# Optimization experiments

Hardware: AMD Instinct MI355X
Metric: run time of the kernel (lower is better)

## Reference

```python
import jax, jax.numpy as jnp
import numpy as np
from jax import lax

DN = ('NCHW', 'OIHW', 'NCHW')


def _conv(x, w, stride, pad):
    return lax.conv_general_dilated(
        x, w, window_strides=(stride, stride),
        padding=((pad, pad), (pad, pad)), dimension_numbers=DN)


def _deconv(x, w):
    # PyTorch ConvTranspose2d(k=4, s=2, p=1): input dilation 2, pad k-1-p=2 -> doubles H,W
    return lax.conv_general_dilated(
        x, w, window_strides=(1, 1), padding=((2, 2), (2, 2)),
        lhs_dilation=(2, 2), dimension_numbers=DN)


def setup_inputs() -> dict:
    key = jax.random.key(0)
    ks = jax.random.split(key, 10)
    B, H, W = 32, 256, 256
    K, E, HID = 512, 64, 128
    s = 0.05
    return {
        'x': jax.random.normal(ks[0], (B, 3, H, W), jnp.float32),
        'enc_w1': jax.random.normal(ks[1], (HID, 3, 4, 4), jnp.float32) * s,
        'enc_b1': jnp.zeros((HID,), jnp.float32),
        'enc_w2': jax.random.normal(ks[2], (E, HID, 4, 4), jnp.float32) * s,
        'enc_b2': jnp.zeros((E,), jnp.float32),
        'dec_w1': jax.random.normal(ks[3], (HID, E, 4, 4), jnp.float32) * s,
        'dec_b1': jnp.zeros((HID,), jnp.float32),
        'dec_w2': jax.random.normal(ks[4], (3, HID, 4, 4), jnp.float32) * s,
        'dec_b2': jnp.zeros((3,), jnp.float32),
        'codebook': jax.random.uniform(ks[5], (K, E), jnp.float32,
                                       minval=-1.0 / K, maxval=1.0 / K),
    }


def reference(x, enc_w1, enc_b1, enc_w2, enc_b2,
              dec_w1, dec_b1, dec_w2, dec_b2, codebook):
    h1 = jax.nn.relu(_conv(x, enc_w1, 2, 1) + enc_b1[None, :, None, None])
    z = _conv(h1, enc_w2, 2, 1) + enc_b2[None, :, None, None]  # [b, e, h, w]

    # ---- vector quantization (faithful to torch reshape order) ----
    b, c, h, w = z.shape
    e = codebook.shape[1]
    zf = z.reshape(b, -1, e)  # [b, n, e] with n = c*h*w/e (c == e -> n = h*w)
    # squared L2 to all codes via quadratic expansion (argmin identical to sqrt-dist)
    d2 = ((zf * zf).sum(-1)[..., None]
          - 2.0 * jnp.einsum('bne,ke->bnk', zf, codebook)
          + (codebook * codebook).sum(-1)[None, None, :])  # [b, n, K]
    idx = jnp.argmin(d2, axis=-1)                            # [b, n]
    z_q = codebook[idx].transpose(0, 2, 1).reshape(-1, e, h, w)  # [b, e, h, w]

    # ---- straight-through estimator ----
    z_q_st = z + lax.stop_gradient(z_q - z)

    d1 = jax.nn.relu(_deconv(z_q_st, dec_w1) + dec_b1[None, :, None, None])
    out = _deconv(d1, dec_w2) + dec_b2[None, :, None, None]
    return out
```

## Files before the change

### kernel.cpp

```cpp
#include <hip/hip_runtime.h>


__device__ int g_isbf;

__device__ __forceinline__ float ldin(const void* p, long long i, int isbf) {
  if (isbf) {
    unsigned v = ((const unsigned short*)p)[i];
    return __uint_as_float(v << 16);
  }
  return ((const float*)p)[i];
}

__device__ __forceinline__ unsigned short f2bf(float f) {
  unsigned u = __float_as_uint(f);
  u += 0x7FFFu + ((u >> 16) & 1u);
  return (unsigned short)(u >> 16);
}

__device__ __forceinline__ float tree64(const float* a) {
  float m[16], u[8], v[4];
#pragma unroll
  for (int l = 0; l < 16; ++l)
    m[l] = __fadd_rn(__fadd_rn(a[l], a[l + 16]), __fadd_rn(a[l + 32], a[l + 48]));
#pragma unroll
  for (int l = 0; l < 8; ++l) u[l] = __fadd_rn(m[l], m[l + 8]);
#pragma unroll
  for (int l = 0; l < 4; ++l) v[l] = __fadd_rn(u[l], u[l + 4]);
  return __fadd_rn(__fadd_rn(v[0], v[2]), __fadd_rn(v[1], v[3]));
}

#define O_W1F   0
#define O_W2T   6144
#define O_DWT2  137216
#define O_DW2T2 268288
#define O_CB    276480
#define O_CN3   309248
#define O_B1    310272
#define O_B2    310400
#define O_DB1   310464
#define O_DB2   310592
#define HDRF    310608
#define PF      1048576
#define PERB    1064960

__global__ void VQVAE_31525059952911_kernel() {}

__global__ __launch_bounds__(256) void k_detect(const unsigned* __restrict__ x) {
  __shared__ int red[256];
  int t = threadIdx.x;
  int cnt = 0;
  for (int i = t; i < 2048; i += 256) {
    unsigned h = x[i] & 0xFFFFu;
    unsigned e = (h >> 7) & 0xFFu;
    if (e >= 100u && e <= 140u) cnt++;
  }
  red[t] = cnt;
  __syncthreads();
  for (int s = 128; s > 0; s >>= 1) {
    if (t < s) red[t] += red[t + s];
    __syncthreads();
  }
  if (t == 0) g_isbf = (red[0] > 1024) ? 1 : 0;
}

__global__ __launch_bounds__(256) void k_prep(
    const void* __restrict__ w1, const void* __restrict__ b1,
    const void* __restrict__ w2, const void* __restrict__ b2,
    const void* __restrict__ dw1, const void* __restrict__ db1,
    const void* __restrict__ dw2, const void* __restrict__ db2,
    const void* __restrict__ cb, float* __restrict__ ws) {
  const int isbf = g_isbf;
  int id = blockIdx.x * 256 + threadIdx.x;
  if (id < 6144) { ws[O_W1F + id] = ldin(w1, id, isbf); return; }
  id -= 6144;
  if (id < 131072) {
    int ci = id >> 10, tap = (id >> 6) & 15, o = id & 63;
    ws[O_W2T + id] = ldin(w2, (o * 128 + ci) * 16 + tap, isbf);
    return;
  }
  id -= 131072;
  if (id < 131072) {
    int r = id & 3, tap = (id >> 2) & 15, ci = (id >> 6) & 63, q = id >> 12;
    ws[O_DWT2 + id] = ldin(dw1, ((q * 4 + r) * 64 + ci) * 16 + tap, isbf);
    return;
  }
  id -= 131072;
  if (id < 8192) {
    int o = id & 3, tap = (id >> 2) & 15, cil = (id >> 6) & 3, cc = id >> 8;
    ws[O_DW2T2 + id] = (o < 3) ? ldin(dw2, (o * 128 + cc * 4 + cil) * 16 + tap, isbf) : 0.f;
    return;
  }
  id -= 8192;
  if (id < 32768) { ws[O_CB + id] = ldin(cb, id, isbf); return; }
  id -= 32768;
  if (id < 512) {
    float q[64];
    for (int d = 0; d < 64; ++d) {
      float v = ldin(cb, id * 64 + d, isbf);
      q[d] = __fmul_rn(v, v);
    }
    ws[O_CN3 + id] = tree64(q);
    return;
  }
  id -= 512;
  if (id < 128) { ws[O_B1 + id] = ldin(b1, id, isbf); return; }
  id -= 128;
  if (id < 64) { ws[O_B2 + id] = ldin(b2, id, isbf); return; }
  id -= 64;
  if (id < 128) { ws[O_DB1 + id] = ldin(db1, id, isbf); return; }
  id -= 4 + 124;
  if (id < 4) { ws[O_DB2 + id] = (id < 3) ? ldin(db2, id, isbf) : 0.f; return; }
}

__global__ __launch_bounds__(256) void k_pproj(
    const void* __restrict__ dw1, const void* __restrict__ cb,
    float* __restrict__ P) {
  __shared__ float cbs[64];
  const int isbf = g_isbf;
  const int t = threadIdx.x;
  const int k = blockIdx.x;
  if (t < 64) cbs[t] = ldin(cb, (long long)k * 64 + t, isbf);
  __syncthreads();
  const int oc = t & 127;
  const int th = t >> 7;
  float acc[8];
#pragma unroll
  for (int j = 0; j < 8; ++j) acc[j] = 0.f;
  for (int ci = 0; ci < 64; ++ci) {
    const float v = cbs[ci];
    const long long base = ((long long)oc * 64 + ci) * 16 + th * 8;
    float wv[8];
    if (isbf) {
      const uint4 raw = *(const uint4*)((const unsigned short*)dw1 + base);
      wv[0] = __uint_as_float((raw.x & 0xFFFFu) << 16);
      wv[1] = __uint_as_float(raw.x & 0xFFFF0000u);
      wv[2] = __uint_as_float((raw.y & 0xFFFFu) << 16);
      wv[3] = __uint_as_float(raw.y & 0xFFFF0000u);
      wv[4] = __uint_as_float((raw.z & 0xFFFFu) << 16);
      wv[5] = __uint_as_float(raw.z & 0xFFFF0000u);
      wv[6] = __uint_as_float((raw.w & 0xFFFFu) << 16);
      wv[7] = __uint_as_float(raw.w & 0xFFFF0000u);
    } else {
      const float4 a = *(const float4*)((const float*)dw1 + base);
      const float4 b = *(const float4*)((const float*)dw1 + base + 4);
      wv[0] = a.x; wv[1] = a.y; wv[2] = a.z; wv[3] = a.w;
      wv[4] = b.x; wv[5] = b.y; wv[6] = b.z; wv[7] = b.w;
    }
#pragma unroll
    for (int j = 0; j < 8; ++j) acc[j] = fmaf(v, wv[j], acc[j]);
  }
#pragma unroll
  for (int j = 0; j < 8; ++j)
    P[(k << 11) + ((th * 8 + j) << 7) + oc] = acc[j];
}

__global__ __launch_bounds__(256) void k_enc(
    const void* __restrict__ x, const float* __restrict__ w1f,
    const float* __restrict__ w2t, const float* __restrict__ b1,
    const float* __restrict__ b2, float* __restrict__ z, int b0) {
  __shared__ float x_s[3][38][38];
  __shared__ float w2_s[8192];
  __shared__ float w1c_s[384];
  __shared__ float h1_s[8][18][18];
  __shared__ float b2_s[64];
  __shared__ float b1c_s[8];
  const int isbf = g_isbf;
  const int t = threadIdx.x;
  const int bz = blockIdx.z, y0 = blockIdx.y * 8, x0 = blockIdx.x * 8;
  const long long xbase = (long long)(b0 + bz) * 3 * 65536;
  for (int i = t; i < 4332; i += 256) {
    int ci = i / 1444, rem = i % 1444, lr = rem / 38, lc = rem % 38;
    int iy = 4 * y0 - 3 + lr, ix = 4 * x0 - 3 + lc;
    float v = 0.f;
    if (iy >= 0 && iy < 256 && ix >= 0 && ix < 256)
      v = ldin(x, xbase + (long long)ci * 65536 + iy * 256 + ix, isbf);
    x_s[ci][lr][lc] = v;
  }
  if (t < 64) b2_s[t] = b2[t];
  const int co0 = (t >> 4) * 4;
  const int pg = t & 15, py = pg & 7, px0 = (pg >> 3) * 4;
  float acc[4][4];
#pragma unroll
  for (int c = 0; c < 4; ++c)
#pragma unroll
    for (int u = 0; u < 4; ++u) acc[c][u] = 0.f;
  for (int cc = 0; cc < 16; ++cc) {
    __syncthreads();
    for (int i = t; i < 8192; i += 256) w2_s[i] = w2t[cc * 8192 + i];
    for (int i = t; i < 384; i += 256) w1c_s[i] = w1f[cc * 384 + i];
    if (t < 8) b1c_s[t] = b1[cc * 8 + t];
    __syncthreads();
    for (int j = t; j < 2592; j += 256) {
      int c = j / 324, rem = j % 324, ly = rem / 18, lx = rem % 18;
      int hy = 2 * y0 - 1 + ly, hx = 2 * x0 - 1 + lx;
      float v = 0.f;
      if (hy >= 0 && hy < 128 && hx >= 0 && hx < 128) {
        const float* wc = &w1c_s[c * 48];
        float a = 0.f;
        for (int ci = 0; ci < 3; ++ci) {
#pragma unroll
          for (int ky = 0; ky < 4; ++ky) {
            const float* xr = &x_s[ci][2 * ly + ky][2 * lx];
            const float* wr = &wc[ci * 16 + ky * 4];
            a = __fadd_rn(a, __fmul_rn(xr[0], wr[0]));
            a = __fadd_rn(a, __fmul_rn(xr[1], wr[1]));
            a = __fadd_rn(a, __fmul_rn(xr[2], wr[2]));
            a = __fadd_rn(a, __fmul_rn(xr[3], wr[3]));
          }
        }
        v = __fadd_rn(a, b1c_s[c]);
        if (v < 0.f) v = 0.f;
      }
      h1_s[c][ly][lx] = v;
    }
    __syncthreads();
    for (int ci = 0; ci < 8; ++ci) {
#pragma unroll
      for (int ky = 0; ky < 4; ++ky) {
        float xrow[10];
#pragma unroll
        for (int q = 0; q < 10; ++q) xrow[q] = h1_s[ci][2 * py + ky][2 * px0 + q];
#pragma unroll
        for (int kx = 0; kx < 4; ++kx) {
          const float* wp = &w2_s[(ci * 16 + ky * 4 + kx) * 64 + co0];
#pragma unroll
          for (int u = 0; u < 4; ++u) {
            const float xv = xrow[2 * u + kx];
            acc[0][u] = __fadd_rn(acc[0][u], __fmul_rn(xv, wp[0]));
            acc[1][u] = __fadd_rn(acc[1][u], __fmul_rn(xv, wp[1]));
            acc[2][u] = __fadd_rn(acc[2][u], __fmul_rn(xv, wp[2]));
            acc[3][u] = __fadd_rn(acc[3][u], __fmul_rn(xv, wp[3]));
          }
        }
      }
    }
  }
  const long long zb = (long long)bz * 262144;
#pragma unroll
  for (int u = 0; u < 4; ++u) {
    long long pos = (long long)(y0 + py) * 64 + x0 + px0 + u;
#pragma unroll
    for (int c = 0; c < 4; ++c)
      z[zb + (long long)(co0 + c) * 4096 + pos] = __fadd_rn(acc[c][u], b2_s[co0 + c]);
  }
}

__global__ __launch_bounds__(256) void k_vq(
    const float* __restrict__ z, const float* __restrict__ cb32,
    const float* __restrict__ cn3, int* __restrict__ idx) {
  __shared__ float cb_s[8192];
  __shared__ float cn_s[128];
  const int t = threadIdx.x;
  const long long g = (long long)blockIdx.x * 256 + t;
  float zr[64], q[64];
  for (int d = 0; d < 64; ++d) zr[d] = z[g * 64 + d];
#pragma unroll
  for (int d = 0; d < 64; ++d) q[d] = __fmul_rn(zr[d], zr[d]);
  const float t1 = tree64(q);
  float best = 3.4e38f;
  int bi = 0;
  for (int ch = 0; ch < 4; ++ch) {
    __syncthreads();
    for (int i = t; i < 8192; i += 256) cb_s[i] = cb32[ch * 8192 + i];
    if (t < 128) cn_s[t] = cn3[ch * 128 + t];
    __syncthreads();
    for (int kl = 0; kl < 128; ++kl) {
      const float* cp = &cb_s[kl * 64];
      float p[64];
#pragma unroll
      for (int d = 0; d < 64; ++d) p[d] = __fmul_rn(zr[d], cp[d]);
      const float t2 = tree64(p);
      const float d2 = __fadd_rn(__fsub_rn(t1, __fmul_rn(2.0f, t2)), cn_s[kl]);
      const int k = ch * 128 + kl;
      if (d2 < best) { best = d2; bi = k; }
    }
  }
  idx[g] = bi;
}

__global__ __launch_bounds__(256) void k_dec(
    const int* __restrict__ idxp, const float* __restrict__ P,
    const float* __restrict__ w2t, const float* __restrict__ db1,
    const float* __restrict__ db2, void* __restrict__ outp, int b0) {
  __shared__ int idx_s[6][18];
  __shared__ float d1_s[4][10][35];
  __shared__ float w2c_s[256];
  __shared__ float db1_s[128];
  const int isbf = g_isbf;
  const int t = threadIdx.x;
  const int bz = blockIdx.z, Y0 = blockIdx.y * 16, X0 = blockIdx.x * 64;
  const int yb = (Y0 >> 2) - 1, xb = (X0 >> 2) - 1;
  if (t < 128) db1_s[t] = db1[t];
  for (int j = t; j < 108; j += 256) {
    int r = j / 18, c = j % 18;
    int yin = yb + r, xin = xb + c;
    int k = -1;
    if (yin >= 0 && yin < 64 && xin >= 0 && xin < 64)
      k = idxp[bz * 4096 + yin * 64 + xin];
    idx_s[r][c] = k;
  }
  const int py = t >> 4, px0 = (t & 15) * 4;
  const int ry = py & 1;
  float acc[3][4];
  for (int o = 0; o < 3; ++o)
    for (int e = 0; e < 4; ++e) acc[o][e] = 0.f;
  for (int cc = 0; cc < 32; ++cc) {
    __syncthreads();
    w2c_s[t] = w2t[cc * 256 + t];
    for (int j = t; j < 340; j += 256) {
      int ldy = j / 34, ldx = j % 34;
      int dy = (Y0 >> 1) - 1 + ldy, dx = (X0 >> 1) - 1 + ldx;
      float s0 = 0.f, s1 = 0.f, s2 = 0.f, s3 = 0.f;
      bool inb = (dy >= 0 && dy < 128 && dx >= 0 && dx < 128);
      if (inb) {
        const int kyp = (ldy + 1) & 1, kxp = (ldx + 1) & 1;
        const int lr0 = (ldy + kyp - 1) >> 1, lc0 = (ldx + kxp - 1) >> 1;
#pragma unroll
        for (int sy = 0; sy < 2; ++sy) {
#pragma unroll
          for (int sx = 0; sx < 2; ++sx) {
            const int k = idx_s[lr0 + sy][lc0 + sx];
            if (k >= 0) {
              const int tap = (kyp + 2 * sy) * 4 + (kxp + 2 * sx);
              const float4 pv =
                  *(const float4*)(P + (k << 11) + (tap << 7) + (cc << 2));
              s0 += pv.x; s1 += pv.y; s2 += pv.z; s3 += pv.w;
            }
          }
        }
        s0 += db1_s[cc * 4 + 0]; if (s0 < 0.f) s0 = 0.f;
        s1 += db1_s[cc * 4 + 1]; if (s1 < 0.f) s1 = 0.f;
        s2 += db1_s[cc * 4 + 2]; if (s2 < 0.f) s2 = 0.f;
        s3 += db1_s[cc * 4 + 3]; if (s3 < 0.f) s3 = 0.f;
      }
      d1_s[0][ldy][ldx] = s0;
      d1_s[1][ldy][ldx] = s1;
      d1_s[2][ldy][ldx] = s2;
      d1_s[3][ldy][ldx] = s3;
    }
    __syncthreads();
    for (int cl = 0; cl < 4; ++cl) {
#pragma unroll
      for (int sy = 0; sy < 2; ++sy) {
        const int ldy = ((py + ry) >> 1) + sy;
#pragma unroll
        for (int sx = 0; sx < 2; ++sx) {
#pragma unroll
          for (int rx = 0; rx < 2; ++rx) {
            const int tap = (ry + 2 * sy) * 4 + rx + 2 * sx;
            const float4 w = *(const float4*)&w2c_s[(cl * 16 + tap) * 4];
#pragma unroll
            for (int ex = 0; ex < 2; ++ex) {
              const int e = 2 * ex + rx;
              const int ldx = ((px0 + e + rx) >> 1) + sx;
              const float dv = d1_s[cl][ldy][ldx];
              acc[0][e] = fmaf(dv, w.x, acc[0][e]);
              acc[1][e] = fmaf(dv, w.y, acc[1][e]);
              acc[2][e] = fmaf(dv, w.z, acc[2][e]);
            }
          }
        }
      }
    }
  }
  const int oy = Y0 + py;
  for (int o = 0; o < 3; ++o) {
    const float bv = db2[o];
    const long long ob = (((long long)(b0 + bz) * 3 + o) * 256 + oy) * 256 + X0 + px0;
    if (isbf) {
      unsigned short* o16 = (unsigned short*)outp;
      for (int e = 0; e < 4; ++e) o16[ob + e] = f2bf(acc[o][e] + bv);
    } else {
      float* o32 = (float*)outp;
      for (int e = 0; e < 4; ++e) o32[ob + e] = acc[o][e] + bv;
    }
  }
}

__global__ __launch_bounds__(256) void k_deco(
    const int* __restrict__ idxp, const float* __restrict__ cb32,
    const float* __restrict__ dwt2, const float* __restrict__ dw2t2,
    const float* __restrict__ db1, const float* __restrict__ db2,
    void* __restrict__ outp, int b0) {
  __shared__ float zq_s[64][6][18];
  __shared__ float w1c_s[4096];
  __shared__ float w2c_s[256];
  __shared__ float d1_s[4][10][34];
  __shared__ float db1_s[128];
  const int isbf = g_isbf;
  const int t = threadIdx.x;
  const int bz = blockIdx.z, Y0 = blockIdx.y * 16, X0 = blockIdx.x * 64;
  const int yb = (Y0 >> 2) - 1, xb = (X0 >> 2) - 1;
  if (t < 128) db1_s[t] = db1[t];
  for (int j = t; j < 6912; j += 256) {
    int ci = j / 108, p = j % 108, r = p / 18, c = p % 18;
    int yin = yb + r, xin = xb + c;
    float v = 0.f;
    if (yin >= 0 && yin < 64 && xin >= 0 && xin < 64) {
      int k = idxp[bz * 4096 + yin * 64 + xin];
      v = cb32[k * 64 + ci];
    }
    zq_s[ci][r][c] = v;
  }
  const int py = t >> 4, px0 = (t & 15) * 4;
  const int ry = py & 1;
  float acc[3][4];
  for (int o = 0; o < 3; ++o)
    for (int e = 0; e < 4; ++e) acc[o][e] = 0.f;
  for (int cc = 0; cc < 32; ++cc) {
    __syncthreads();
    for (int i = t; i < 4096; i += 256) w1c_s[i] = dwt2[cc * 4096 + i];
    if (t < 256) w2c_s[t] = dw2t2[cc * 256 + t];
    __syncthreads();
    for (int j = t; j < 1360; j += 256) {
      int ocl = j / 340, p = j % 340, ldy = p / 34, ldx = p % 34;
      int dy = (Y0 >> 1) - 1 + ldy, dx = (X0 >> 1) - 1 + ldx;
      float val = 0.f;
      if (dy >= 0 && dy < 128 && dx >= 0 && dx < 128) {
        const int kyp = (ldy + 1) & 1, kxp = (ldx + 1) & 1;
        const int lr0 = (ldy + kyp - 1) >> 1, lc0 = (ldx + kxp - 1) >> 1;
        float s = 0.f;
#pragma unroll
        for (int sy = 0; sy < 2; ++sy) {
#pragma unroll
          for (int sx = 0; sx < 2; ++sx) {
            const int tap = (kyp + 2 * sy) * 4 + (kxp + 2 * sx);
            const int lr = lr0 + sy, lc = lc0 + sx;
            const float* wp = &w1c_s[tap * 4 + ocl];
            float ss = 0.f;
            for (int ci = 0; ci < 64; ++ci)
              ss = fmaf(zq_s[ci][lr][lc], wp[ci * 64], ss);
            s += ss;
          }
        }
        val = s + db1_s[cc * 4 + ocl];
        if (val < 0.f) val = 0.f;
      }
      d1_s[ocl][ldy][ldx] = val;
    }
    __syncthreads();
    for (int cl = 0; cl < 4; ++cl) {
#pragma unroll
      for (int e = 0; e < 4; ++e) {
        const int rx = e & 1;
#pragma unroll
        for (int sy = 0; sy < 2; ++sy) {
          const int ky = ry + 2 * sy;
          const int ldy = ((py + ry) >> 1) + sy;
#pragma unroll
          for (int sx = 0; sx < 2; ++sx) {
            const int kx = rx + 2 * sx;
            const int ldx = ((px0 + e + rx) >> 1) + sx;
            const float dv = d1_s[cl][ldy][ldx];
            const float* wp = &w2c_s[(cl * 16 + ky * 4 + kx) * 4];
            acc[0][e] = fmaf(dv, wp[0], acc[0][e]);
            acc[1][e] = fmaf(dv, wp[1], acc[1][e]);
            acc[2][e] = fmaf(dv, wp[2], acc[2][e]);
          }
        }
      }
    }
  }
  const int oy = Y0 + py;
  for (int o = 0; o < 3; ++o) {
    const float bv = db2[o];
    const long long ob = (((long long)(b0 + bz) * 3 + o) * 256 + oy) * 256 + X0 + px0;
    if (isbf) {
      unsigned short* o16 = (unsigned short*)outp;
      for (int e = 0; e < 4; ++e) o16[ob + e] = f2bf(acc[o][e] + bv);
    } else {
      float* o32 = (float*)outp;
      for (int e = 0; e < 4; ++e) o32[ob + e] = acc[o][e] + bv;
    }
  }
}

static void run_chunk_p(const void* x, float* hdr, float* P, float* zb, int* ib,
                        void* out, int C, int b0, hipStream_t stream) {
  dim3 ge(8, 8, C);
  k_enc<<<ge, 256, 0, stream>>>(x, hdr + O_W1F, hdr + O_W2T, hdr + O_B1,
                                hdr + O_B2, zb, b0);
  k_vq<<<16 * C, 256, 0, stream>>>(zb, hdr + O_CB, hdr + O_CN3, ib);
  dim3 gd(4, 16, C);
  k_dec<<<gd, 256, 0, stream>>>(ib, P, hdr + O_DW2T2, hdr + O_DB1,
                                hdr + O_DB2, out, b0);
}

static void run_chunk_o(const void* x, float* hdr, float* zb, int* ib, void* out,
                        int C, int b0, hipStream_t stream) {
  dim3 ge(8, 8, C);
  k_enc<<<ge, 256, 0, stream>>>(x, hdr + O_W1F, hdr + O_W2T, hdr + O_B1,
                                hdr + O_B2, zb, b0);
  k_vq<<<16 * C, 256, 0, stream>>>(zb, hdr + O_CB, hdr + O_CN3, ib);
  dim3 gd(4, 16, C);
  k_deco<<<gd, 256, 0, stream>>>(ib, hdr + O_CB, hdr + O_DWT2, hdr + O_DW2T2,
                                 hdr + O_DB1, hdr + O_DB2, out, b0);
}

extern "C" void kernel_launch(void* const* d_in, const int* in_sizes, int n_in,
                              void* d_out, int out_size, void* d_ws, size_t ws_size,
                              hipStream_t stream) {
  (void)out_size;
  const void *x = 0, *w1 = 0, *b1 = 0, *w2 = 0, *b2 = 0;
  const void *dw1 = 0, *db1 = 0, *dw2 = 0, *db2 = 0, *cb = 0;
  static const int dictsz[10] = {6291456, 6144, 128, 131072, 64, 131072, 128, 6144, 3, 32768};
  int isdict = 1;
  if (n_in >= 10) {
    for (int i = 0; i < 10; ++i)
      if (in_sizes[i] != dictsz[i]) isdict = 0;
  } else isdict = 0;
  if (isdict) {
    x = d_in[0]; w1 = d_in[1]; b1 = d_in[2]; w2 = d_in[3]; b2 = d_in[4];
    dw1 = d_in[5]; db1 = d_in[6]; dw2 = d_in[7]; db2 = d_in[8]; cb = d_in[9];
  } else {
    int c6144 = 0, c131072 = 0, c128 = 0;
    for (int i = 0; i < n_in; ++i) {
      switch (in_sizes[i]) {
        case 6291456: x = d_in[i]; break;
        case 32768: cb = d_in[i]; break;
        case 64: b2 = d_in[i]; break;
        case 3: db2 = d_in[i]; break;
        case 6144: if (c6144++ == 0) w1 = d_in[i]; else dw2 = d_in[i]; break;
        case 131072: if (c131072++ == 0) w2 = d_in[i]; else dw1 = d_in[i]; break;
        case 128: if (c128++ == 0) b1 = d_in[i]; else db1 = d_in[i]; break;
        default: break;
      }
    }
    if (!x || !w1 || !b1 || !w2 || !b2 || !dw1 || !db1 || !dw2 || !db2 || !cb) {
      x = d_in[0]; w1 = d_in[1]; b1 = d_in[2]; w2 = d_in[3]; b2 = d_in[4];
      dw1 = d_in[5]; db1 = d_in[6]; dw2 = d_in[7]; db2 = d_in[8]; cb = d_in[9];
    }
  }

  k_detect<<<1, 256, 0, stream>>>((const unsigned*)x);

  const size_t HDRB = (size_t)HDRF * 4;
  const size_t HDR2F = (size_t)HDRF + (size_t)PF;
  const size_t HDR2B = HDR2F * 4;

  if (ws_size >= HDR2B + (size_t)PERB) {
    int C = 32;
    while (C > 1 && HDR2B + (size_t)C * PERB > ws_size) C >>= 1;
    float* hdr = (float*)d_ws;
    float* P = hdr + HDRF;
    float* zb = hdr + HDR2F;
    int* ib = (int*)((char*)zb + (size_t)C * 1048576);
    k_prep<<<1212, 256, 0, stream>>>(w1, b1, w2, b2, dw1, db1, dw2, db2, cb, hdr);
    k_pproj<<<512, 256, 0, stream>>>(dw1, cb, P);
    for (int b0 = 0; b0 < 32; b0 += C)
      run_chunk_p(x, hdr, P, zb, ib, d_out, C, b0, stream);
  } else {
    {
      float* SA = (float*)d_out;
      float* zb = SA + HDRF;
      int* ib = (int*)((char*)zb + 1048576);
      k_prep<<<1212, 256, 0, stream>>>(w1, b1, w2, b2, dw1, db1, dw2, db2, cb, SA);
      for (int i = 31; i >= 6; --i) run_chunk_o(x, SA, zb, ib, d_out, 1, i, stream);
    }
    {
      float* SB = (float*)((char*)x + 10275520);
      float* zb = SB + HDRF;
      int* ib = (int*)((char*)zb + 1048576);
      k_prep<<<1212, 256, 0, stream>>>(w1, b1, w2, b2, dw1, db1, dw2, db2, cb, SB);
      for (int i = 5; i >= 0; --i) run_chunk_o(x, SB, zb, ib, d_out, 1, i, stream);
    }
  }
}
```

Before: 1.654 ms.

## Shrink encoder channel chunk, pad LDS, and register-block h1 computation

Halves the per-iteration hidden-channel chunk in the fused encoder from 8 to 4, which roughly halves shared memory, and adds a launch-bounds hint so more blocks can be resident per CU. Each thread now computes three adjacent h1 outputs per row and reuses the loaded input values across them. The x tile is padded to reduce bank conflicts, and w2 weights are read as float4. The price is twice as many outer iterations and barriers, and the register cap may force spills.

```diff
diff --git a/kernel.cpp b/kernel.cpp
--- a/kernel.cpp
+++ b/kernel.cpp
@@ -154,16 +154,16 @@
     P[(k << 11) + ((th * 8 + j) << 7) + oc] = acc[j];
 }
 
-__global__ __launch_bounds__(256) void k_enc(
+__global__ __launch_bounds__(256, 4) void k_enc(
     const void* __restrict__ x, const float* __restrict__ w1f,
     const float* __restrict__ w2t, const float* __restrict__ b1,
     const float* __restrict__ b2, float* __restrict__ z, int b0) {
-  __shared__ float x_s[3][38][38];
-  __shared__ float w2_s[8192];
-  __shared__ float w1c_s[384];
-  __shared__ float h1_s[8][18][18];
+  __shared__ float x_s[3][38][39];
+  __shared__ float w2_s[4096];
+  __shared__ float w1c_s[192];
+  __shared__ float h1_s[4][18][18];
   __shared__ float b2_s[64];
-  __shared__ float b1c_s[8];
+  __shared__ float b1c_s[4];
   const int isbf = g_isbf;
   const int t = threadIdx.x;
   const int bz = blockIdx.z, y0 = blockIdx.y * 8, x0 = blockIdx.x * 8;
@@ -184,37 +184,62 @@
   for (int c = 0; c < 4; ++c)
 #pragma unroll
     for (int u = 0; u < 4; ++u) acc[c][u] = 0.f;
-  for (int cc = 0; cc < 16; ++cc) {
-    __syncthreads();
-    for (int i = t; i < 8192; i += 256) w2_s[i] = w2t[cc * 8192 + i];
-    for (int i = t; i < 384; i += 256) w1c_s[i] = w1f[cc * 384 + i];
-    if (t < 8) b1c_s[t] = b1[cc * 8 + t];
-    __syncthreads();
-    for (int j = t; j < 2592; j += 256) {
-      int c = j / 324, rem = j % 324, ly = rem / 18, lx = rem % 18;
-      int hy = 2 * y0 - 1 + ly, hx = 2 * x0 - 1 + lx;
-      float v = 0.f;
-      if (hy >= 0 && hy < 128 && hx >= 0 && hx < 128) {
+  for (int cc = 0; cc < 32; ++cc) {
+    __syncthreads();
+    for (int i = t; i < 4096; i += 256) w2_s[i] = w2t[cc * 4096 + i];
+    if (t < 192) w1c_s[t] = w1f[cc * 192 + t];
+    if (t < 4) b1c_s[t] = b1[cc * 4 + t];
+    __syncthreads();
+    for (int s = t; s < 432; s += 256) {
+      const int c = s / 108, rs = s % 108;
+      const int ly = rs / 6, lx0 = (rs % 6) * 3;
+      const int hy = 2 * y0 - 1 + ly;
+      const int hx0 = 2 * x0 - 1 + lx0;
+      float a0 = 0.f, a1 = 0.f, a2 = 0.f;
+      const bool rowok = (hy >= 0 && hy < 128);
+      if (rowok) {
         const float* wc = &w1c_s[c * 48];
-        float a = 0.f;
+#pragma unroll
         for (int ci = 0; ci < 3; ++ci) {
 #pragma unroll
           for (int ky = 0; ky < 4; ++ky) {
-            const float* xr = &x_s[ci][2 * ly + ky][2 * lx];
+            const float* xr = &x_s[ci][2 * ly + ky][2 * lx0];
+            const float x0r = xr[0], x1r = xr[1], x2r = xr[2], x3r = xr[3];
+            const float x4r = xr[4], x5r = xr[5], x6r = xr[6], x7r = xr[7];
             const float* wr = &wc[ci * 16 + ky * 4];
-            a = __fadd_rn(a, __fmul_rn(xr[0], wr[0]));
-            a = __fadd_rn(a, __fmul_rn(xr[1], wr[1]));
-            a = __fadd_rn(a, __fmul_rn(xr[2], wr[2]));
-            a = __fadd_rn(a, __fmul_rn(xr[3], wr[3]));
+            const float w0 = wr[0], w1 = wr[1], w2 = wr[2], w3 = wr[3];
+            a0 = __fadd_rn(a0, __fmul_rn(x0r, w0));
+            a1 = __fadd_rn(a1, __fmul_rn(x2r, w0));
+            a2 = __fadd_rn(a2, __fmul_rn(x4r, w0));
+            a0 = __fadd_rn(a0, __fmul_rn(x1r, w1));
+            a1 = __fadd_rn(a1, __fmul_rn(x3r, w1));
+            a2 = __fadd_rn(a2, __fmul_rn(x5r, w1));
+            a0 = __fadd_rn(a0, __fmul_rn(x2r, w2));
+            a1 = __fadd_rn(a1, __fmul_rn(x4r, w2));
+            a2 = __fadd_rn(a2, __fmul_rn(x6r, w2));
+            a0 = __fadd_rn(a0, __fmul_rn(x3r, w3));
+            a1 = __fadd_rn(a1, __fmul_rn(x5r, w3));
+            a2 = __fadd_rn(a2, __fmul_rn(x7r, w3));
           }
         }
-        v = __fadd_rn(a, b1c_s[c]);
-        if (v < 0.f) v = 0.f;
-      }
-      h1_s[c][ly][lx] = v;
-    }
-    __syncthreads();
-    for (int ci = 0; ci < 8; ++ci) {
+      }
+      float v0 = 0.f, v1 = 0.f, v2 = 0.f;
+      if (rowok) {
+        const float bb = b1c_s[c];
+        v0 = __fadd_rn(a0, bb); if (v0 < 0.f) v0 = 0.f;
+        v1 = __fadd_rn(a1, bb); if (v1 < 0.f) v1 = 0.f;
+        v2 = __fadd_rn(a2, bb); if (v2 < 0.f) v2 = 0.f;
+        if (hx0 < 0) v0 = 0.f;
+        if (hx0 >= 128) v0 = 0.f;
+        if (hx0 + 1 >= 128) v1 = 0.f;
+        if (hx0 + 2 >= 128) v2 = 0.f;
+      }
+      h1_s[c][ly][lx0] = v0;
+      h1_s[c][ly][lx0 + 1] = v1;
+      h1_s[c][ly][lx0 + 2] = v2;
+    }
+    __syncthreads();
+    for (int ci = 0; ci < 4; ++ci) {
 #pragma unroll
       for (int ky = 0; ky < 4; ++ky) {
         float xrow[10];
@@ -222,14 +247,14 @@
         for (int q = 0; q < 10; ++q) xrow[q] = h1_s[ci][2 * py + ky][2 * px0 + q];
 #pragma unroll
         for (int kx = 0; kx < 4; ++kx) {
-          const float* wp = &w2_s[(ci * 16 + ky * 4 + kx) * 64 + co0];
+          const float4 w = *(const float4*)&w2_s[(ci * 16 + ky * 4 + kx) * 64 + co0];
 #pragma unroll
           for (int u = 0; u < 4; ++u) {
             const float xv = xrow[2 * u + kx];
-            acc[0][u] = __fadd_rn(acc[0][u], __fmul_rn(xv, wp[0]));
-            acc[1][u] = __fadd_rn(acc[1][u], __fmul_rn(xv, wp[1]));
-            acc[2][u] = __fadd_rn(acc[2][u], __fmul_rn(xv, wp[2]));
-            acc[3][u] = __fadd_rn(acc[3][u], __fmul_rn(xv, wp[3]));
+            acc[0][u] = __fadd_rn(acc[0][u], __fmul_rn(xv, w.x));
+            acc[1][u] = __fadd_rn(acc[1][u], __fmul_rn(xv, w.y));
+            acc[2][u] = __fadd_rn(acc[2][u], __fmul_rn(xv, w.z));
+            acc[3][u] = __fadd_rn(acc[3][u], __fmul_rn(xv, w.w));
           }
         }
       }
```

Result: faster. 1.478 ms (-10.7%).
